# Kernel tuning notes

Measured on AMD Instinct MI355X. Metric: run time of the kernel, lower is better.

Reference implementation:

```python
import jax, jax.numpy as jnp
import numpy as np

UNITS = 300
MDN_MIXES = 8  # Config.mdn_mixes: 3*8=24 MDN params + 1 length = 25-dim feedback
FEAT = 25
GATE_IN = 2 * FEAT  # concat(inputs, prev_output)


def setup_inputs() -> dict:
    key = jax.random.key(0)
    ks = jax.random.split(key, 12)
    B, T = 2048, 512
    x = jax.random.uniform(ks[0], (B, T, FEAT), dtype=jnp.float32)
    s = 0.05
    kernel = jax.random.normal(ks[1], (FEAT, 4 * UNITS), dtype=jnp.float32) * s
    recurrent_kernel = jax.random.normal(ks[2], (UNITS, 4 * UNITS), dtype=jnp.float32) * s
    # unit_forget_bias: zeros except forget-gate slice = ones
    bias = jnp.concatenate([
        jnp.zeros((UNITS,), jnp.float32),
        jnp.ones((UNITS,), jnp.float32),
        jnp.zeros((2 * UNITS,), jnp.float32),
    ])
    # MLPGate: 2-layer MLP combining the two 25-dim distributions -> 24-dim
    mlp_w1 = jax.random.normal(ks[3], (GATE_IN, GATE_IN), dtype=jnp.float32) * s
    mlp_b1 = jnp.zeros((GATE_IN,), jnp.float32)
    mlp_w2 = jax.random.normal(ks[4], (GATE_IN, FEAT - 1), dtype=jnp.float32) * s
    mlp_b2 = jnp.zeros((FEAT - 1,), jnp.float32)
    # MDN heads on h (units -> mdn_mixes each)
    wa = jax.random.normal(ks[5], (UNITS, MDN_MIXES), dtype=jnp.float32) * s
    ba = jnp.zeros((MDN_MIXES,), jnp.float32)
    wm = jax.random.normal(ks[6], (UNITS, MDN_MIXES), dtype=jnp.float32) * s
    bm = jnp.zeros((MDN_MIXES,), jnp.float32)
    ws = jax.random.normal(ks[7], (UNITS, MDN_MIXES), dtype=jnp.float32) * s
    bs = jnp.zeros((MDN_MIXES,), jnp.float32)
    return {
        'x': x, 'kernel': kernel, 'recurrent_kernel': recurrent_kernel, 'bias': bias,
        'mlp_w1': mlp_w1, 'mlp_b1': mlp_b1, 'mlp_w2': mlp_w2, 'mlp_b2': mlp_b2,
        'wa': wa, 'ba': ba, 'wm': wm, 'bm': bm, 'ws': ws, 'bs': bs,
    }


def _hard_sigmoid(z):
    return jnp.clip(0.2 * z + 0.5, 0.0, 1.0)


def _nnelu(z):
    return 1.0 + jax.nn.elu(z)


def reference(x, kernel, recurrent_kernel, bias,
              mlp_w1, mlp_b1, mlp_w2, mlp_b2,
              wa, ba, wm, bm, ws, bs):
    B = x.shape[0]
    dt = x.dtype

    def step(carry, xt):
        h, c, prev = carry  # [B,U], [B,U], [B,25]
        il = xt[:, 24:25]
        pl = prev[:, 24:25]
        combined = il + pl
        denom = jnp.maximum(combined, jnp.asarray(1e-8, dt))  # LengthNormalizer
        inp2 = jnp.concatenate([xt[:, :24], il / denom], axis=1)
        prev2 = jnp.concatenate([prev[:, :24], pl / denom], axis=1)
        # MLP gate combining the two distributions
        g = jax.nn.relu(jnp.concatenate([inp2, prev2], axis=1) @ mlp_w1 + mlp_b1)
        g = g @ mlp_w2 + mlp_b2  # [B,24]
        gate_out = jnp.concatenate([g, combined], axis=1)  # [B,25]
        # LSTM gates (split-kernel math == fused without dropout)
        z = gate_out @ kernel + h @ recurrent_kernel + bias  # [B,4U]
        zi, zf, zc, zo = jnp.split(z, 4, axis=1)
        i = _hard_sigmoid(zi)
        f = _hard_sigmoid(zf)
        o = _hard_sigmoid(zo)
        c_new = f * c + i * jnp.tanh(zc)
        h_new = o * jnp.tanh(c_new)
        # MDN heads
        alpha = jax.nn.softmax(h_new @ wa + ba, axis=-1)
        mu = h_new @ wm + bm
        sigma = _nnelu(h_new @ ws + bs)
        mdn = jnp.concatenate([alpha, mu, sigma, combined], axis=1)  # [B,25]
        return (h_new, c_new, mdn), mdn

    h0 = jnp.zeros((B, UNITS), dt)
    c0 = jnp.zeros((B, UNITS), dt)
    prev0 = jnp.zeros((B, FEAT), dt)
    xt = jnp.swapaxes(x, 0, 1)  # [T,B,25]
    _, ys = jax.lax.scan(step, (h0, c0, prev0), xt)
    return jnp.swapaxes(ys, 0, 1)  # [B,T,25]
```

## Files before the change

### kernel.cpp

```cpp
#include <hip/hip_runtime.h>
#include <math.h>

#define BB 2048
#define TT 512
#define NFEAT 25
#define UNITS 300
#define RPB 16
#define NBLK (BB/RPB)
#define NT 1024
#define NW 16
#define NKS 11
#define TPW 5
#define HROW 360
#define F8ROW 392
#define G2ROW 40
#define GROW 72

#define OFF_M1 0
#define SZ_M1  (4*2*512)
#define OFF_M2 (OFF_M1 + SZ_M1)
#define SZ_M2  (2*2*512)
#define OFF_H  (OFF_M2 + SZ_M2)
#define SZ_H   (2*NKS*512)
#define OFF_BZ (OFF_H + SZ_H)
#define OFF_WK (OFF_BZ + 2560)
#define OFF_B08 (OFF_WK + 2560)
#define SZ_B08B (NW*TPW*512)
#define OFF_F8 (OFF_B08 + 20480)
#define SZ_F8B (NW*10*TPW*512)
#define SW_SZ  (SZ_M1 + SZ_M2 + SZ_H)
#define SWM1   0
#define SWM2   (SZ_M1)
#define SWH    (SZ_M1 + SZ_M2)

typedef __attribute__((ext_vector_type(4))) float f32x4;
typedef __attribute__((ext_vector_type(8))) short bf16x8;
typedef long long ll8;

static __device__ __forceinline__ unsigned short f2bf(float f) {
    union { float f; unsigned u; } x; x.f = f;
    unsigned r = (x.u + 0x7fffu + ((x.u >> 16) & 1u)) >> 16;
    return (unsigned short)r;
}
static __device__ __forceinline__ unsigned char f2f8(float f) {
    return (unsigned char)(__builtin_amdgcn_cvt_pk_fp8_f32(f, 0.f, 0, false) & 0xff);
}
static __device__ __forceinline__ float ftanh(float v) {
    float e = __builtin_amdgcn_exp2f(v * 2.8853900817779268f);
    return 1.f - 2.f * __builtin_amdgcn_rcpf(e + 1.f);
}
static __device__ __forceinline__ int zcol(int c) { return (c & 3) * 300 + (c >> 2); }

#define BARRIER() asm volatile("s_waitcnt lgkmcnt(0)\n\ts_barrier" ::: "memory")

__global__ __launch_bounds__(256) void conv_b08(
    const float* __restrict__ wk, unsigned char* __restrict__ dst8)
{
    int idx = blockIdx.x * 256 + threadIdx.x;
    if (idx >= SZ_B08B) return;
    int j = idx & 7, n = (idx >> 3) & 15, kg = (idx >> 7) & 3, q = idx >> 9;
    int i = q % TPW, w = q / TPW;
    int k = kg * 8 + j, c = (w + NW * i) * 16 + n;
    float v = (k < 24 && c < 1200) ? wk[k * 1200 + zcol(c)] : 0.f;
    dst8[idx] = f2f8(v);
}

__global__ __launch_bounds__(256) void conv_b8(
    const float* __restrict__ wr, unsigned char* __restrict__ dst8)
{
    int idx = blockIdx.x * 256 + threadIdx.x;
    if (idx >= SZ_F8B) return;
    int j = idx & 7, n = (idx >> 3) & 15, kg = (idx >> 7) & 3, q = idx >> 9;
    int i = q % TPW, ks1 = (q / TPW) % 10, w = q / (TPW * 10);
    int k = (ks1 + 1) * 32 + kg * 8 + j, c = (w + NW * i) * 16 + n;
    float v = (k >= 32 && k < 332 && c < 1200) ? wr[(k - 32) * 1200 + zcol(c)] : 0.f;
    dst8[idx] = f2f8(v);
}

__global__ __launch_bounds__(256) void conv_misc(
    const float* __restrict__ wk, const float* __restrict__ bz,
    float* __restrict__ bzdst, float* __restrict__ wkdst)
{
    int i = blockIdx.x * 256 + threadIdx.x;
    if (i >= 1280) return;
    float vb = 0.f, vw = 0.f;
    if (i < 1200) {
        int oc = zcol(i);
        vb = bz[oc];
        vw = wk[24 * 1200 + oc];
    }
    bzdst[i] = vb;
    wkdst[i] = vw;
}

__global__ __launch_bounds__(256) void conv_gen(
    const float* __restrict__ W, unsigned short* __restrict__ dst,
    int K, int N, int nks, int total)
{
    int idx = blockIdx.x * 256 + threadIdx.x;
    if (idx >= total) return;
    int j = idx & 7, n = (idx >> 3) & 15, kg = (idx >> 7) & 3, qq = idx >> 9;
    int ks = qq % nks, nt = qq / nks;
    int k = ks * 32 + kg * 8 + j, col = nt * 16 + n;
    float v = (k < K && col < N) ? W[k * N + col] : 0.f;
    dst[idx] = f2bf(v);
}

__global__ __launch_bounds__(256) void conv_heads(
    const float* __restrict__ wa, const float* __restrict__ wm,
    const float* __restrict__ wsg, const float* __restrict__ ba,
    const float* __restrict__ bm, const float* __restrict__ bs,
    unsigned short* __restrict__ dst)
{
    int idx = blockIdx.x * 256 + threadIdx.x;
    if (idx >= SZ_H) return;
    int j = idx & 7, n = (idx >> 3) & 15, kg = (idx >> 7) & 3, qq = idx >> 9;
    int ks = qq % NKS, nt = qq / NKS;
    int k = ks * 32 + kg * 8 + j, col = nt * 16 + n;
    float v = 0.f;
    if (col < 24) {
        if (k >= 32 && k < 332) {
            int u = k - 32, h = col >> 3, m = col & 7;
            const float* W = (h == 0) ? wa : (h == 1) ? wm : wsg;
            v = W[u * 8 + m];
        } else if (k == 332) {
            v = (col < 8) ? ba[col] : (col < 16) ? bm[col - 8] : bs[col - 16];
        }
    }
    dst[idx] = f2bf(v);
}

#define MFMA   __builtin_amdgcn_mfma_f32_16x16x32_bf16
#define MFMA8  __builtin_amdgcn_mfma_f32_16x16x32_fp8_fp8
#define LOG2E  1.4426950408889634f

__global__ __launch_bounds__(NT)
void dilstm(
    const float* __restrict__ x,
    const unsigned short* __restrict__ wf,
    const float* __restrict__ b1v,
    const float* __restrict__ b2v,
    float* __restrict__ out)
{
    __shared__ unsigned short Hbf[RPB][HROW];
    __shared__ __attribute__((aligned(16))) unsigned char Af8[2][RPB][F8ROW];
    __shared__ __attribute__((aligned(16))) unsigned char G2b8[RPB][G2ROW];
    __shared__ unsigned short Gbf[RPB][GROW];
    __shared__ unsigned short G1b[RPB][GROW];
    __shared__ float Sc[RPB][24];
    __shared__ float Sc2[RPB][24];
    __shared__ float BzS[1280];
    __shared__ float WkS[1280];
    __shared__ float CombS[RPB];
    __shared__ float Zw[NW][2][16][20];
    __shared__ unsigned short SW[SW_SZ];

    const int t = threadIdx.x;
    const int lane = t & 63, wv = t >> 6;
    const int arow = lane & 15, akg = lane >> 4;
    const int crow0 = akg * 4;
    const int u_l = lane & 3, rr = lane >> 2;
    const int row0 = blockIdx.x * RPB;

    for (int i = t; i < RPB * HROW; i += NT) ((unsigned short*)Hbf)[i] = 0;
    for (int i = t; i < 2 * RPB * F8ROW; i += NT) ((unsigned char*)Af8)[i] = 0;
    for (int i = t; i < RPB * G2ROW; i += NT) ((unsigned char*)G2b8)[i] = 0;
    for (int i = t; i < RPB * GROW; i += NT) { ((unsigned short*)Gbf)[i] = 0; ((unsigned short*)G1b)[i] = 0; }
    for (int i = t; i < SW_SZ; i += NT) SW[i] = wf[OFF_M1 + i];
    {
        const float* bzp = (const float*)(wf + OFF_BZ);
        const float* wkp = (const float*)(wf + OFF_WK);
        for (int i = t; i < 1280; i += NT) { BzS[i] = bzp[i]; WkS[i] = wkp[i]; }
    }
    if (t < RPB) Hbf[t][332] = f2bf(1.f);

    float m1bias = 0.f, m2bias = 0.f;
    {
        int c1 = (wv & 3) * 16 + arow;
        if (wv < 4 && c1 < 50) m1bias = b1v[c1];
        if (wv < 2 && c1 < 24) m2bias = b2v[c1];
    }

    float creg[TPW];
    #pragma unroll
    for (int i = 0; i < TPW; ++i) creg[i] = 0.f;

    const unsigned char* bw08 = (const unsigned char*)(wf + OFF_B08) + wv * (TPW * 512) + (lane << 3);
    const unsigned char* bw8  = (const unsigned char*)(wf + OFF_F8) + (size_t)wv * (10 * TPW * 512) + (lane << 3);

    const int rA = t / 25, eA = t - (t / 25) * 25;
    float combreg = 0.f, xreg = 0.f;
    if (t < RPB * NFEAT) xreg = x[((size_t)(row0 + rA) * TT) * NFEAT + eA];
    __syncthreads();

    if (t < RPB * NFEAT) {
        if (eA < 24) {
            Gbf[rA][eA] = f2bf(xreg);
        } else {
            float comb = xreg;
            combreg = comb;
            float denom = fmaxf(comb, 1e-8f);
            Gbf[rA][24] = f2bf(xreg / denom);
            CombS[rA] = comb;
        }
    }
    __syncthreads();

    for (int ts = 0; ts < TT; ++ts) {
        const int p = ts & 1;

        ll8 b08[TPW], bbA[TPW];
        #pragma unroll
        for (int i = 0; i < TPW; ++i)
            b08[i] = *(const ll8*)(bw08 + i * 512);
        #pragma unroll
        for (int i = 0; i < TPW; ++i)
            bbA[i] = *(const ll8*)(bw8 + i * 512);
        if (t < RPB * NFEAT && ts + 1 < TT)
            xreg = x[((size_t)(row0 + rA) * TT + (ts + 1)) * NFEAT + eA];

        if (wv < 4) {
            bf16x8 a0 = *(const bf16x8*)&Gbf[arow][akg * 8];
            bf16x8 a1 = *(const bf16x8*)&Gbf[arow][32 + akg * 8];
            bf16x8 b0 = *(const bf16x8*)&SW[SWM1 + (wv * 2 + 0) * 512 + (lane << 3)];
            bf16x8 b1 = *(const bf16x8*)&SW[SWM1 + (wv * 2 + 1) * 512 + (lane << 3)];
            f32x4 acc1 = {0.f, 0.f, 0.f, 0.f};
            acc1 = MFMA(a0, b0, acc1, 0, 0, 0);
            acc1 = MFMA(a1, b1, acc1, 0, 0, 0);
            int col = wv * 16 + arow;
            if (col < 50) {
                #pragma unroll
                for (int rg = 0; rg < 4; ++rg)
                    G1b[crow0 + rg][col] = f2bf(fmaxf(acc1[rg] + m1bias, 0.f));
            }
        }
        BARRIER();

        if (wv < 2) {
            bf16x8 a0 = *(const bf16x8*)&G1b[arow][akg * 8];
            bf16x8 a1 = *(const bf16x8*)&G1b[arow][32 + akg * 8];
            bf16x8 b0 = *(const bf16x8*)&SW[SWM2 + (wv * 2 + 0) * 512 + (lane << 3)];
            bf16x8 b1 = *(const bf16x8*)&SW[SWM2 + (wv * 2 + 1) * 512 + (lane << 3)];
            f32x4 acc2 = {0.f, 0.f, 0.f, 0.f};
            acc2 = MFMA(a0, b0, acc2, 0, 0, 0);
            acc2 = MFMA(a1, b1, acc2, 0, 0, 0);
            int col = wv * 16 + arow;
            if (col < 24) {
                #pragma unroll
                for (int rg = 0; rg < 4; ++rg)
                    G2b8[crow0 + rg][col] = f2f8(acc2[rg] + m2bias);
            }
        }
        BARRIER();

        {
            f32x4 acc[TPW];
            #pragma unroll
            for (int i = 0; i < TPW; ++i) acc[i] = (f32x4){0.f, 0.f, 0.f, 0.f};

            {
                ll8 a8g = *(const ll8*)&G2b8[arow][akg * 8];
                #pragma unroll
                for (int i = 0; i < TPW; ++i)
                    acc[i] = MFMA8(a8g, b08[i], acc[i], 0, 0, 0);
            }
            {
                const unsigned char* af8p = &Af8[p][0][0] + arow * F8ROW + akg * 8;
                const unsigned char* bp = bw8;
                ll8 bbB[TPW];
                #pragma unroll 1
                for (int pr = 0; pr < 5; ++pr) {
                    const int ks = 2 * pr + 1;
                    ll8 a8a = *(const ll8*)(af8p + ks * 32);
                    ll8 a8b = *(const ll8*)(af8p + ks * 32 + 32);
                    #pragma unroll
                    for (int i = 0; i < TPW; ++i)
                        bbB[i] = *(const ll8*)(bp + 2560 + i * 512);
                    #pragma unroll
                    for (int i = 0; i < TPW; ++i)
                        acc[i] = MFMA8(a8a, bbA[i], acc[i], 0, 0, 0);
                    if (pr < 4) {
                        #pragma unroll
                        for (int i = 0; i < TPW; ++i)
                            bbA[i] = *(const ll8*)(bp + 5120 + i * 512);
                    }
                    #pragma unroll
                    for (int i = 0; i < TPW; ++i)
                        acc[i] = MFMA8(a8b, bbB[i], acc[i], 0, 0, 0);
                    bp += 5120;
                }
            }

            float cmb = CombS[rr];
            #pragma unroll
            for (int rg = 0; rg < 4; ++rg)
                Zw[wv][0][crow0 + rg][arow] = acc[0][rg];
            #pragma unroll
            for (int i = 0; i < TPW; ++i) {
                if (i + 1 < TPW) {
                    #pragma unroll
                    for (int rg = 0; rg < 4; ++rg)
                        Zw[wv][(i + 1) & 1][crow0 + rg][arow] = acc[i + 1][rg];
                }
                f32x4 bz4 = *(const f32x4*)&BzS[(wv + NW * i) * 16 + 4 * u_l];
                f32x4 wk4 = *(const f32x4*)&WkS[(wv + NW * i) * 16 + 4 * u_l];
                f32x4 z4  = *(const f32x4*)&Zw[wv][i & 1][rr][4 * u_l];
                float zi = z4[0] + bz4[0] + cmb * wk4[0];
                float zf = z4[1] + bz4[1] + cmb * wk4[1];
                float zc = z4[2] + bz4[2] + cmb * wk4[2];
                float zo = z4[3] + bz4[3] + cmb * wk4[3];
                if (wv + NW * i < 75) {
                    float ig = fminf(fmaxf(0.2f * zi + 0.5f, 0.f), 1.f);
                    float fg = fminf(fmaxf(0.2f * zf + 0.5f, 0.f), 1.f);
                    float og = fminf(fmaxf(0.2f * zo + 0.5f, 0.f), 1.f);
                    float cn = fg * creg[i] + ig * ftanh(zc);
                    creg[i] = cn;
                    float hn = og * ftanh(cn);
                    int hb = (wv + NW * i) * 4 + u_l;
                    Hbf[rr][32 + hb] = f2bf(hn);
                    Af8[p ^ 1][rr][32 + hb] = f2f8(hn);
                }
            }
        }
        BARRIER();

        if (wv < 4) {
            const int ct = wv & 1, half = wv >> 1;
            const int k0 = 1 + 5 * half;
            bf16x8 ah[5];
            #pragma unroll
            for (int q = 0; q < 5; ++q)
                ah[q] = *(const bf16x8*)&Hbf[arow][(k0 + q) * 32 + akg * 8];
            f32x4 acc3 = {0.f, 0.f, 0.f, 0.f};
            #pragma unroll
            for (int q = 0; q < 5; ++q) {
                bf16x8 b = *(const bf16x8*)&SW[SWH + (ct * NKS + k0 + q) * 512 + (lane << 3)];
                acc3 = MFMA(ah[q], b, acc3, 0, 0, 0);
            }
            int col = ct * 16 + arow;
            if (col < 24) {
                if (half == 0) {
                    #pragma unroll
                    for (int rg = 0; rg < 4; ++rg)
                        Sc[crow0 + rg][col] = acc3[rg];
                } else {
                    #pragma unroll
                    for (int rg = 0; rg < 4; ++rg)
                        Sc2[crow0 + rg][col] = acc3[rg];
                }
            }
        }
        BARRIER();

        if (t < RPB * NFEAT) {
            float v;
            if (eA < 8) {
                float s0 = Sc[rA][0] + Sc2[rA][0];
                float mx = s0;
                float sv[8]; sv[0] = s0;
                #pragma unroll
                for (int m = 1; m < 8; ++m) {
                    sv[m] = Sc[rA][m] + Sc2[rA][m];
                    mx = fmaxf(mx, sv[m]);
                }
                float sum = 0.f;
                #pragma unroll
                for (int m = 0; m < 8; ++m)
                    sum += __builtin_amdgcn_exp2f((sv[m] - mx) * LOG2E);
                v = __builtin_amdgcn_exp2f((sv[eA] - mx) * LOG2E) / sum;
            } else if (eA < 16) {
                v = Sc[rA][eA] + Sc2[rA][eA];
            } else if (eA < 24) {
                float s = Sc[rA][eA] + Sc2[rA][eA];
                v = (s > 0.f) ? (1.f + s) : __builtin_amdgcn_exp2f(s * LOG2E);
            } else {
                v = combreg;
            }
            out[((size_t)(row0 + rA) * TT + ts) * NFEAT + eA] = v;
            if (eA < 24) {
                Gbf[rA][eA]      = f2bf(xreg);
                Gbf[rA][25 + eA] = f2bf(v);
            } else {
                float comb = xreg + combreg;
                float denom = fmaxf(comb, 1e-8f);
                Gbf[rA][24] = f2bf(xreg / denom);
                Gbf[rA][49] = f2bf(combreg / denom);
                CombS[rA] = comb;
                combreg = comb;
            }
        }
        BARRIER();
    }
}

extern "C" void kernel_launch(void* const* d_in, const int* in_sizes, int n_in,
                              void* d_out, int out_size, void* d_ws, size_t ws_size,
                              hipStream_t stream) {
    const float* x   = (const float*)d_in[0];
    const float* wk  = (const float*)d_in[1];
    const float* wr  = (const float*)d_in[2];
    const float* bz  = (const float*)d_in[3];
    const float* w1  = (const float*)d_in[4];
    const float* b1  = (const float*)d_in[5];
    const float* w2  = (const float*)d_in[6];
    const float* b2  = (const float*)d_in[7];
    const float* wa  = (const float*)d_in[8];
    const float* ba  = (const float*)d_in[9];
    const float* wm  = (const float*)d_in[10];
    const float* bm  = (const float*)d_in[11];
    const float* wsg = (const float*)d_in[12];
    const float* bs  = (const float*)d_in[13];
    float* out = (float*)d_out;
    unsigned short* wf = (unsigned short*)d_ws;
    unsigned char*  wf08 = (unsigned char*)(wf + OFF_B08);
    unsigned char*  wf8  = (unsigned char*)(wf + OFF_F8);
    float* bzdst = (float*)(wf + OFF_BZ);
    float* wkdst = (float*)(wf + OFF_WK);

    conv_b08<<<(SZ_B08B + 255) / 256, 256, 0, stream>>>(wk, wf08);
    conv_b8<<<(SZ_F8B + 255) / 256, 256, 0, stream>>>(wr, wf8);
    conv_misc<<<(1280 + 255) / 256, 256, 0, stream>>>(wk, bz, bzdst, wkdst);
    conv_gen<<<(SZ_M1 + 255) / 256, 256, 0, stream>>>(w1, wf + OFF_M1, 50, 50, 2, SZ_M1);
    conv_gen<<<(SZ_M2 + 255) / 256, 256, 0, stream>>>(w2, wf + OFF_M2, 50, 24, 2, SZ_M2);
    conv_heads<<<(SZ_H + 255) / 256, 256, 0, stream>>>(wa, wm, wsg, ba, bm, bs, wf + OFF_H);
    dilstm<<<NBLK, NT, 0, stream>>>(x, wf, b1, b2, out);
}
```

Before: 3.619 ms.

## Spread recurrent FP8 MFMA k-slices across barrier phases and halve waves per block

Each block now runs 8 waves instead of 16, so every wave owns 10 gate tiles instead of 5, and launch bounds ask for two blocks per CU. The recurrent h·W MFMA k-slices are split into pairs and issued inside the otherwise idle phases of the step: the MDN head, output writeback and the two MLP-gate stages. Only the input-gate MFMA remains on the critical path before the LSTM cell update. Accumulators and the first B-fragment registers now live across loop iterations. The aim is to hide the long recurrent matmul behind the serial small-GEMM phases and barriers, at the cost of much higher register pressure and possible spills.

After: 9.816 ms. 2.71x slower.

```diff
diff --git a/kernel.cpp b/kernel.cpp
--- a/kernel.cpp
+++ b/kernel.cpp
@@ -7,10 +7,10 @@
 #define UNITS 300
 #define RPB 16
 #define NBLK (BB/RPB)
-#define NT 1024
-#define NW 16
+#define NT 512
+#define NW 8
 #define NKS 11
-#define TPW 5
+#define TPW 10
 #define HROW 360
 #define F8ROW 392
 #define G2ROW 40
@@ -134,7 +134,29 @@
 #define MFMA8  __builtin_amdgcn_mfma_f32_16x16x32_fp8_fp8
 #define LOG2E  1.4426950408889634f
 
-__global__ __launch_bounds__(NT)
+#define KSPAIR(KSA, PP, LOADNEXT) do {                                        \
+    const unsigned char* bp_ = bw8 + ((KSA) - 1) * (TPW * 512);               \
+    const unsigned char* af_ = &Af8[PP][0][0] + arow * F8ROW + akg * 8;       \
+    ll8 bbB_[TPW];                                                            \
+    _Pragma("unroll")                                                         \
+    for (int i = 0; i < TPW; ++i)                                             \
+        bbB_[i] = *(const ll8*)(bp_ + (TPW * 512) + i * 512);                 \
+    ll8 a8a_ = *(const ll8*)(af_ + (KSA) * 32);                               \
+    _Pragma("unroll")                                                         \
+    for (int i = 0; i < TPW; ++i)                                             \
+        acc[i] = MFMA8(a8a_, bbA[i], acc[i], 0, 0, 0);                        \
+    if (LOADNEXT) {                                                           \
+        _Pragma("unroll")                                                     \
+        for (int i = 0; i < TPW; ++i)                                         \
+            bbA[i] = *(const ll8*)(bp_ + 2 * (TPW * 512) + i * 512);          \
+    }                                                                         \
+    ll8 a8b_ = *(const ll8*)(af_ + ((KSA) + 1) * 32);                         \
+    _Pragma("unroll")                                                         \
+    for (int i = 0; i < TPW; ++i)                                             \
+        acc[i] = MFMA8(a8b_, bbB_[i], acc[i], 0, 0, 0);                       \
+} while (0)
+
+__global__ __launch_bounds__(NT, 2)
 void dilstm(
     const float* __restrict__ x,
     const unsigned short* __restrict__ wf,
@@ -176,7 +198,7 @@
 
     float m1bias = 0.f, m2bias = 0.f;
     {
-        int c1 = (wv & 3) * 16 + arow;
+        int c1 = wv * 16 + arow;
         if (wv < 4 && c1 < 50) m1bias = b1v[c1];
         if (wv < 2 && c1 < 24) m2bias = b2v[c1];
     }
@@ -186,7 +208,15 @@
     for (int i = 0; i < TPW; ++i) creg[i] = 0.f;
 
     const unsigned char* bw08 = (const unsigned char*)(wf + OFF_B08) + wv * (TPW * 512) + (lane << 3);
-    const unsigned char* bw8  = (const unsigned char*)(wf + OFF_F8) + (size_t)wv * (10 * TPW * 512) + (lane << 3);
+    const unsigned char* bw8  = (const unsigned char*)(wf + OFF_F8) + (size_t)wv * (100 * 512) + (lane << 3);
+
+    f32x4 acc[TPW];
+    #pragma unroll
+    for (int i = 0; i < TPW; ++i) acc[i] = (f32x4){0.f, 0.f, 0.f, 0.f};
+    ll8 bbA[TPW];
+    #pragma unroll
+    for (int i = 0; i < TPW; ++i)
+        bbA[i] = *(const ll8*)(bw8 + 6 * (TPW * 512) + i * 512);
 
     const int rA = t / 25, eA = t - (t / 25) * 25;
     float combreg = 0.f, xreg = 0.f;
@@ -209,23 +239,15 @@
     for (int ts = 0; ts < TT; ++ts) {
         const int p = ts & 1;
 
-        ll8 b08[TPW], bbA[TPW];
-        #pragma unroll
-        for (int i = 0; i < TPW; ++i)
-            b08[i] = *(const ll8*)(bw08 + i * 512);
-        #pragma unroll
-        for (int i = 0; i < TPW; ++i)
-            bbA[i] = *(const ll8*)(bw8 + i * 512);
         if (t < RPB * NFEAT && ts + 1 < TT)
             xreg = x[((size_t)(row0 + rA) * TT + (ts + 1)) * NFEAT + eA];
-
         if (wv < 4) {
             bf16x8 a0 = *(const bf16x8*)&Gbf[arow][akg * 8];
             bf16x8 a1 = *(const bf16x8*)&Gbf[arow][32 + akg * 8];
             bf16x8 b0 = *(const bf16x8*)&SW[SWM1 + (wv * 2 + 0) * 512 + (lane << 3)];
-            bf16x8 b1 = *(const bf16x8*)&SW[SWM1 + (wv * 2 + 1) * 512 + (lane << 3)];
             f32x4 acc1 = {0.f, 0.f, 0.f, 0.f};
             acc1 = MFMA(a0, b0, acc1, 0, 0, 0);
+            bf16x8 b1 = *(const bf16x8*)&SW[SWM1 + (wv * 2 + 1) * 512 + (lane << 3)];
             acc1 = MFMA(a1, b1, acc1, 0, 0, 0);
             int col = wv * 16 + arow;
             if (col < 50) {
@@ -234,15 +256,16 @@
                     G1b[crow0 + rg][col] = f2bf(fmaxf(acc1[rg] + m1bias, 0.f));
             }
         }
+        KSPAIR(7, p, 1);
         BARRIER();
 
         if (wv < 2) {
             bf16x8 a0 = *(const bf16x8*)&G1b[arow][akg * 8];
             bf16x8 a1 = *(const bf16x8*)&G1b[arow][32 + akg * 8];
             bf16x8 b0 = *(const bf16x8*)&SW[SWM2 + (wv * 2 + 0) * 512 + (lane << 3)];
-            bf16x8 b1 = *(const bf16x8*)&SW[SWM2 + (wv * 2 + 1) * 512 + (lane << 3)];
             f32x4 acc2 = {0.f, 0.f, 0.f, 0.f};
             acc2 = MFMA(a0, b0, acc2, 0, 0, 0);
+            bf16x8 b1 = *(const bf16x8*)&SW[SWM2 + (wv * 2 + 1) * 512 + (lane << 3)];
             acc2 = MFMA(a1, b1, acc2, 0, 0, 0);
             int col = wv * 16 + arow;
             if (col < 24) {
@@ -251,45 +274,22 @@
                     G2b8[crow0 + rg][col] = f2f8(acc2[rg] + m2bias);
             }
         }
+        KSPAIR(9, p, 0);
         BARRIER();
 
         {
-            f32x4 acc[TPW];
-            #pragma unroll
-            for (int i = 0; i < TPW; ++i) acc[i] = (f32x4){0.f, 0.f, 0.f, 0.f};
-
-            {
-                ll8 a8g = *(const ll8*)&G2b8[arow][akg * 8];
-                #pragma unroll
-                for (int i = 0; i < TPW; ++i)
-                    acc[i] = MFMA8(a8g, b08[i], acc[i], 0, 0, 0);
-            }
-            {
-                const unsigned char* af8p = &Af8[p][0][0] + arow * F8ROW + akg * 8;
-                const unsigned char* bp = bw8;
-                ll8 bbB[TPW];
-                #pragma unroll 1
-                for (int pr = 0; pr < 5; ++pr) {
-                    const int ks = 2 * pr + 1;
-                    ll8 a8a = *(const ll8*)(af8p + ks * 32);
-                    ll8 a8b = *(const ll8*)(af8p + ks * 32 + 32);
-                    #pragma unroll
-                    for (int i = 0; i < TPW; ++i)
-                        bbB[i] = *(const ll8*)(bp + 2560 + i * 512);
-                    #pragma unroll
-                    for (int i = 0; i < TPW; ++i)
-                        acc[i] = MFMA8(a8a, bbA[i], acc[i], 0, 0, 0);
-                    if (pr < 4) {
-                        #pragma unroll
-                        for (int i = 0; i < TPW; ++i)
-                            bbA[i] = *(const ll8*)(bp + 5120 + i * 512);
-                    }
-                    #pragma unroll
-                    for (int i = 0; i < TPW; ++i)
-                        acc[i] = MFMA8(a8b, bbB[i], acc[i], 0, 0, 0);
-                    bp += 5120;
-                }
-            }
+            ll8 b08[TPW];
+            #pragma unroll
+            for (int i = 0; i < TPW; ++i)
+                b08[i] = *(const ll8*)(bw08 + i * 512);
+            #pragma unroll
+            for (int i = 0; i < TPW; ++i)
+                bbA[i] = *(const ll8*)(bw8 + i * 512);
+
+            ll8 a8g = *(const ll8*)&G2b8[arow][akg * 8];
+            #pragma unroll
+            for (int i = 0; i < TPW; ++i)
+                acc[i] = MFMA8(a8g, b08[i], acc[i], 0, 0, 0);
 
             float cmb = CombS[rr];
             #pragma unroll
@@ -320,6 +320,7 @@
                     Hbf[rr][32 + hb] = f2bf(hn);
                     Af8[p ^ 1][rr][32 + hb] = f2f8(hn);
                 }
+                acc[i] = (f32x4){0.f, 0.f, 0.f, 0.f};
             }
         }
         BARRIER();
@@ -327,15 +328,12 @@
         if (wv < 4) {
             const int ct = wv & 1, half = wv >> 1;
             const int k0 = 1 + 5 * half;
-            bf16x8 ah[5];
-            #pragma unroll
-            for (int q = 0; q < 5; ++q)
-                ah[q] = *(const bf16x8*)&Hbf[arow][(k0 + q) * 32 + akg * 8];
             f32x4 acc3 = {0.f, 0.f, 0.f, 0.f};
             #pragma unroll
             for (int q = 0; q < 5; ++q) {
+                bf16x8 a = *(const bf16x8*)&Hbf[arow][(k0 + q) * 32 + akg * 8];
                 bf16x8 b = *(const bf16x8*)&SW[SWH + (ct * NKS + k0 + q) * 512 + (lane << 3)];
-                acc3 = MFMA(ah[q], b, acc3, 0, 0, 0);
+                acc3 = MFMA(a, b, acc3, 0, 0, 0);
             }
             int col = ct * 16 + arow;
             if (col < 24) {
@@ -350,6 +348,8 @@
                 }
             }
         }
+        KSPAIR(1, p ^ 1, 1);
+        KSPAIR(3, p ^ 1, 1);
         BARRIER();
 
         if (t < RPB * NFEAT) {
@@ -389,6 +389,7 @@
                 combreg = comb;
             }
         }
+        KSPAIR(5, p ^ 1, 1);
         BARRIER();
     }
 }
```
